# Performance work log

Hardware: AMD Instinct MI355X
Metric: run time of the kernel (lower is better)

The kernel has to match this reference:

```python
import jax, jax.numpy as jnp
import numpy as np

D_MODEL = 2048
NUM_HEADS = 16
HEAD_DIM = D_MODEL // NUM_HEADS  # 128
B, L = 2, 2048


def setup_inputs() -> dict:
    key = jax.random.key(0)
    ks = jax.random.split(key, 7)
    s = 0.02
    return {
        "x": jax.random.normal(ks[0], (B, L, D_MODEL), dtype=jnp.float32),
        "Wq_w": jax.random.normal(ks[1], (D_MODEL, D_MODEL), dtype=jnp.float32) * s,
        "Wq_b": jnp.zeros((D_MODEL,), dtype=jnp.float32),
        "Wk_w": jax.random.normal(ks[2], (HEAD_DIM, D_MODEL), dtype=jnp.float32) * s,
        "Wk_b": jnp.zeros((HEAD_DIM,), dtype=jnp.float32),
        "Wv_w": jax.random.normal(ks[3], (HEAD_DIM, D_MODEL), dtype=jnp.float32) * s,
        "Wv_b": jnp.zeros((HEAD_DIM,), dtype=jnp.float32),
    }


def reference(x, Wq_w, Wq_b, Wk_w, Wk_b, Wv_w, Wv_b):
    b, l, _ = x.shape
    # torch Linear: y = x @ W.T + b
    Q = (x @ Wq_w.T + Wq_b).reshape(b, l, NUM_HEADS, HEAD_DIM)  # [B,L,H,D]
    K = x @ Wk_w.T + Wk_b  # [B,L,D] single shared KV head (MQA)
    V = x @ Wv_w.T + Wv_b  # [B,L,D]
    scale = 1.0 / jnp.sqrt(jnp.float32(HEAD_DIM))
    # scores: [B,H,Lq,Lk]; K's head dim (size 1 in torch) broadcasts -> contract over d only
    scores = jnp.einsum("bqhd,bkd->bhqk", Q, K) * scale
    attn = jax.nn.softmax(scores, axis=-1)
    out = jnp.einsum("bhqk,bkd->bqhd", attn, V)  # [B,L,H,D]
    return out.reshape(b, l, D_MODEL)
```

## Files before the change

### kernel.cpp

```cpp
#include <hip/hip_runtime.h>
#include <hip/hip_bf16.h>


typedef unsigned short u16;
typedef unsigned int u32;
typedef __bf16 bf16x8 __attribute__((ext_vector_type(8)));
typedef float f32x16 __attribute__((ext_vector_type(16)));
typedef u16 u16x4 __attribute__((ext_vector_type(4)));
typedef u32 u32x4 __attribute__((ext_vector_type(4)));

#define MFMA32(a, b, c) __builtin_amdgcn_mfma_f32_32x32x16_bf16((a), (b), (c), 0, 0, 0)

__device__ __forceinline__ u16 f2bf(float f) {
  __hip_bfloat16 h = __float2bfloat16(f);
  return __builtin_bit_cast(u16, h);
}

__device__ __forceinline__ float fexp2(float x) {
#if __has_builtin(__builtin_amdgcn_exp2f)
  return __builtin_amdgcn_exp2f(x);
#else
  return exp2f(x);
#endif
}

__device__ __forceinline__ void cp16(const void* g, void* l) {
  __builtin_amdgcn_global_load_lds(
      (const __attribute__((address_space(1))) u32*)g,
      (__attribute__((address_space(3))) u32*)l, 16, 0, 0);
}

__device__ __forceinline__ f32x16 zero16() {
  f32x16 v;
#pragma unroll
  for (int i = 0; i < 16; ++i) v[i] = 0.f;
  return v;
}

__global__ __launch_bounds__(256) void k_convert(
    const float* __restrict__ x, const float* __restrict__ wq,
    const float* __restrict__ wk, const float* __restrict__ wv,
    u16* __restrict__ xb, u16* __restrict__ wqb,
    u16* __restrict__ wkb, u16* __restrict__ wvb) {
  int idx = blockIdx.x * 256 + threadIdx.x;
  for (int i = idx; i < 3276800; i += 524288) {
    float4 v; u16* dst;
    if (i < 2097152) {
      v = ((const float4*)x)[i]; dst = xb + (size_t)i * 4;
    } else if (i < 3145728) {
      int j = i - 2097152; v = ((const float4*)wq)[j]; dst = wqb + (size_t)j * 4;
    } else if (i < 3211264) {
      int j = i - 3145728; v = ((const float4*)wk)[j]; dst = wkb + (size_t)j * 4;
    } else {
      int j = i - 3211264; v = ((const float4*)wv)[j]; dst = wvb + (size_t)j * 4;
    }
    u16x4 o;
    o[0] = f2bf(v.x); o[1] = f2bf(v.y); o[2] = f2bf(v.z); o[3] = f2bf(v.w);
    *(u16x4*)dst = o;
  }
}

__global__ __launch_bounds__(256, 2) void k_gemm_qkv(
    const u16* __restrict__ xb, const u16* __restrict__ wqb,
    const u16* __restrict__ wkb, const u16* __restrict__ wvb,
    const float* __restrict__ bq, const float* __restrict__ bk, const float* __restrict__ bv,
    u16* __restrict__ qout, u16* __restrict__ kout, u16* __restrict__ vtout) {
  __shared__ __align__(16) u16 sh[36864];
  const int tid = threadIdx.x;
  const int w = tid >> 6, lane = tid & 63, ln = lane & 31, hi = lane >> 5;
  const int wr = w >> 1, wc = w & 1;
  const int m0 = blockIdx.x * 128;
  const int by = blockIdx.y;
  const int mode = (by < 16) ? 0 : (by - 15);
  const int n0loc = (mode == 0) ? by * 128 : 0;
  const u16* __restrict__ Bp = (mode == 0) ? wqb : (mode == 1 ? wkb : wvb);
  const u16* Arow = xb + (size_t)m0 * 2048;
  const u16* Brow = Bp + (size_t)n0loc * 2048;

  const u16* sb[9];
#pragma unroll
  for (int i = 0; i < 9; ++i) {
    int s = (w + i * 4) * 64 + lane;
    const u16* base; int r, c;
    if (s < 1152) { r = s / 9; c = s % 9; if (c > 7) c = 0; base = Arow; }
    else { int s2 = s - 1152; r = s2 / 9; c = s2 % 9; if (c > 7) c = 0; base = Brow; }
    sb[i] = base + (size_t)r * 2048 + c * 8;
  }

  f32x16 acc[2][2];
  acc[0][0] = zero16(); acc[0][1] = zero16(); acc[1][0] = zero16(); acc[1][1] = zero16();

  const int a0off = (wr * 64 + ln) * 72 + hi * 8;
  const int b0off = 9216 + (wc * 64 + ln) * 72 + hi * 8;

#pragma unroll
  for (int i = 0; i < 9; ++i)
    cp16(sb[i], (void*)(sh + (w + i * 4) * 512));
  __syncthreads();

  for (int it = 0; it < 32; ++it) {
    const int cur = (it & 1) * 18432;
    const int nxt = 18432 - cur;
    const int k0n = (it < 31) ? (it + 1) * 64 : 0;
#pragma unroll
    for (int i = 0; i < 9; ++i)
      cp16(sb[i] + k0n, (void*)(sh + nxt + (w + i * 4) * 512));

#pragma unroll
    for (int kc = 0; kc < 4; ++kc) {
      const int ko = kc * 16;
      bf16x8 a0 = *(const bf16x8*)&sh[cur + a0off + ko];
      bf16x8 a1 = *(const bf16x8*)&sh[cur + a0off + 2304 + ko];
      bf16x8 b0 = *(const bf16x8*)&sh[cur + b0off + ko];
      bf16x8 b1 = *(const bf16x8*)&sh[cur + b0off + 2304 + ko];
      acc[0][0] = MFMA32(a0, b0, acc[0][0]);
      acc[0][1] = MFMA32(a0, b1, acc[0][1]);
      acc[1][0] = MFMA32(a1, b0, acc[1][0]);
      acc[1][1] = MFMA32(a1, b1, acc[1][1]);
    }

    __syncthreads();
  }

  const float qscale = 0.12751744630098356f;
#pragma unroll
  for (int fm = 0; fm < 2; ++fm) {
#pragma unroll
    for (int fn = 0; fn < 2; ++fn) {
      f32x16 a = acc[fm][fn];
      const int mbase = m0 + wr * 64 + fm * 32;
      const int nloc = n0loc + wc * 64 + fn * 32 + ln;
      if (mode == 0) {
        const float bsc = bq[nloc] * qscale;
#pragma unroll
        for (int r = 0; r < 16; ++r) {
          int row = (r & 3) + 8 * (r >> 2) + 4 * hi;
          qout[(size_t)(mbase + row) * 2048 + nloc] = f2bf(a[r] * qscale + bsc);
        }
      } else if (mode == 1) {
        const float bb = bk[nloc];
#pragma unroll
        for (int r = 0; r < 16; ++r) {
          int row = (r & 3) + 8 * (r >> 2) + 4 * hi;
          kout[(size_t)(mbase + row) * 128 + nloc] = f2bf(a[r] + bb);
        }
      } else {
        const float bb = bv[nloc];
#pragma unroll
        for (int r = 0; r < 16; ++r) {
          int row = (r & 3) + 8 * (r >> 2) + 4 * hi;
          int m = mbase + row;
          vtout[(size_t)((m >> 11) * 128 + nloc) * 2048 + (m & 2047)] = f2bf(a[r] + bb);
        }
      }
    }
  }
}

__global__ __launch_bounds__(512, 2) void k_attn(
    const u16* __restrict__ qb, const u16* __restrict__ kb, const u16* __restrict__ vtb,
    float* __restrict__ out) {
  __shared__ __align__(16) u16 sh[35840];
  const int tid = threadIdx.x;
  const int w = tid >> 6, lane = tid & 63, ln = lane & 31, hi = lane >> 5;
  const int q0 = blockIdx.x * 256, h = blockIdx.y, b = blockIdx.z;
  const size_t bL = (size_t)b * 2048;
  const u16* kbase = kb + bL * 128;
  const u16* vbase = vtb + (size_t)b * 128 * 2048;

  bf16x8 qf[8];
  {
    const u16* qrow = qb + (bL + q0 + w * 32 + ln) * 2048 + h * 128 + hi * 8;
#pragma unroll
    for (int kc = 0; kc < 8; ++kc) qf[kc] = *(const bf16x8*)(qrow + kc * 16);
  }

  const u16* sb[5]; int smul[5];
  const int nsl = (w < 3) ? 5 : 4;
#pragma unroll
  for (int i = 0; i < 5; ++i) {
    int sl = w + i * 8;
    if (sl < 35) {
      int s = sl * 64 + lane;
      if (s < 1088) {
        int r = s / 17, c = s % 17; if (c > 15) c = 0;
        sb[i] = kbase + r * 128 + c * 8; smul[i] = 128;
      } else {
        int s2 = s - 1088; int r = s2 / 9, c = s2 % 9; if (c > 7) c = 0;
        sb[i] = vbase + (size_t)r * 2048 + c * 8; smul[i] = 1;
      }
    } else { sb[i] = kbase; smul[i] = 0; }
  }

#pragma unroll
  for (int i = 0; i < 5; ++i)
    if (i < nsl) cp16(sb[i], (void*)(sh + (w + i * 8) * 512));
  __syncthreads();

  f32x16 o[4];
#pragma unroll
  for (int dg = 0; dg < 4; ++dg) o[dg] = zero16();
  float l = 0.f;

  const int kro = ln * 136 + hi * 8;
  const int vro = 8704 + ln * 72 + hi * 8;

  for (int it = 0; it < 32; ++it) {
    const int cur = (it & 1) * 17920;
    const int nxt = 17920 - cur;
    const size_t k0n = (it < 31) ? (size_t)(it + 1) * 64 : 0;
#pragma unroll
    for (int i = 0; i < 5; ++i)
      if (i < nsl) cp16(sb[i] + k0n * smul[i], (void*)(sh + nxt + (w + i * 8) * 512));

    f32x16 s0 = zero16(), s1 = zero16();
#pragma unroll
    for (int kc = 0; kc < 8; ++kc) {
      bf16x8 a0 = *(const bf16x8*)&sh[cur + kro + kc * 16];
      bf16x8 a1 = *(const bf16x8*)&sh[cur + kro + 32 * 136 + kc * 16];
      s0 = MFMA32(a0, qf[kc], s0);
      s1 = MFMA32(a1, qf[kc], s1);
    }

    u32 pk[16];
#pragma unroll
    for (int i = 0; i < 8; ++i) {
      float a = fexp2(s0[2 * i]), c = fexp2(s0[2 * i + 1]);
      pk[i] = __builtin_amdgcn_perm(__builtin_bit_cast(u32, c),
                                    __builtin_bit_cast(u32, a), 0x07060302u);
      float d = fexp2(s1[2 * i]), e = fexp2(s1[2 * i + 1]);
      pk[8 + i] = __builtin_amdgcn_perm(__builtin_bit_cast(u32, e),
                                        __builtin_bit_cast(u32, d), 0x07060302u);
    }
#pragma unroll
    for (int i = 0; i < 16; ++i) {
      l += __builtin_bit_cast(float, pk[i] << 16);
      l += __builtin_bit_cast(float, pk[i] & 0xffff0000u);
    }

    bf16x8 pf[4];
#pragma unroll
    for (int c = 0; c < 4; ++c) {
      const int wb = 4 * c;
      u32 send0 = hi ? pk[wb] : pk[wb + 2];
      u32 send1 = hi ? pk[wb + 1] : pk[wb + 3];
      u32 r0 = (u32)__shfl_xor((int)send0, 32, 64);
      u32 r1 = (u32)__shfl_xor((int)send1, 32, 64);
      u32x4 v;
      v[0] = hi ? r0 : pk[wb];
      v[1] = hi ? r1 : pk[wb + 1];
      v[2] = hi ? pk[wb + 2] : r0;
      v[3] = hi ? pk[wb + 3] : r1;
      pf[c] = __builtin_bit_cast(bf16x8, v);
    }

#pragma unroll
    for (int c = 0; c < 4; ++c)
#pragma unroll
      for (int dg = 0; dg < 4; ++dg) {
        bf16x8 va = *(const bf16x8*)&sh[cur + vro + dg * 2304 + c * 16];
        o[dg] = MFMA32(va, pf[c], o[dg]);
      }

    __syncthreads();
  }

  l += __shfl_xor(l, 32, 64);
  const float inv = 1.0f / l;

  float* orow = out + (bL + q0 + w * 32 + ln) * 2048 + h * 128 + hi * 4;
#pragma unroll
  for (int dg = 0; dg < 4; ++dg)
#pragma unroll
    for (int rq = 0; rq < 4; ++rq) {
      float4 v4;
      v4.x = o[dg][rq * 4 + 0] * inv; v4.y = o[dg][rq * 4 + 1] * inv;
      v4.z = o[dg][rq * 4 + 2] * inv; v4.w = o[dg][rq * 4 + 3] * inv;
      *(float4*)&orow[dg * 32 + rq * 8] = v4;
    }
}

extern "C" void kernel_launch(void* const* d_in, const int* in_sizes, int n_in,
                              void* d_out, int out_size, void* d_ws, size_t ws_size,
                              hipStream_t stream) {
  const float* x  = (const float*)d_in[0];
  const float* wq = (const float*)d_in[1];
  const float* bq = (const float*)d_in[2];
  const float* wk = (const float*)d_in[3];
  const float* bk = (const float*)d_in[4];
  const float* wv = (const float*)d_in[5];
  const float* bv = (const float*)d_in[6];
  float* out = (float*)d_out;
  char* ws = (char*)d_ws;

  u16* xb   = (u16*)(ws);
  u16* wqb  = (u16*)(ws + 16777216);
  u16* wkb  = (u16*)(ws + 25165824);
  u16* wvb  = (u16*)(ws + 25690112);
  u16* qb   = (u16*)(ws + 26214400);
  u16* kbuf = (u16*)(ws + 42991616);
  u16* vtb  = (u16*)(ws + 44040192);

  k_convert<<<2048, 256, 0, stream>>>(x, wq, wk, wv, xb, wqb, wkb, wvb);
  k_gemm_qkv<<<dim3(32, 18), 256, 0, stream>>>(xb, wqb, wkb, wvb, bq, bk, bv, qb, kbuf, vtb);
  k_attn<<<dim3(8, 16, 2), 512, 0, stream>>>(qb, kbuf, vtb, out);
}
```

Baseline: 229.5 us.

## Halve attention block size, add MFMA priority hints, use permlane32 swap and packed bf16 convert

The attention kernel now launches 256-thread blocks covering 128 query rows each, with twice as many blocks, and each wave issues more cp16 loads to fill the shared K/V tile. s_setprio raises wave priority around the MFMA loops in both the QKV GEMM and attention kernels so matrix issue is favoured over other waves. Softmax packing switches to v_cvt_pk_bf16_f32, which rounds instead of truncating, and the row sum now accumulates the fp32 exponentials rather than the truncated bf16 values. The cross-half shuffle becomes v_permlane32_swap. Smaller blocks mean each K/V tile load to LDS serves fewer queries, trading that extra load traffic for better scheduling flexibility.

```diff
diff --git a/kernel.cpp b/kernel.cpp
--- a/kernel.cpp
+++ b/kernel.cpp
@@ -106,6 +106,7 @@
     for (int i = 0; i < 9; ++i)
       cp16(sb[i] + k0n, (void*)(sh + nxt + (w + i * 4) * 512));
 
+    __builtin_amdgcn_s_setprio(1);
 #pragma unroll
     for (int kc = 0; kc < 4; ++kc) {
       const int ko = kc * 16;
@@ -118,6 +119,7 @@
       acc[1][0] = MFMA32(a1, b0, acc[1][0]);
       acc[1][1] = MFMA32(a1, b1, acc[1][1]);
     }
+    __builtin_amdgcn_s_setprio(0);
 
     __syncthreads();
   }
@@ -157,13 +159,13 @@
   }
 }
 
-__global__ __launch_bounds__(512, 2) void k_attn(
+__global__ __launch_bounds__(256, 2) void k_attn(
     const u16* __restrict__ qb, const u16* __restrict__ kb, const u16* __restrict__ vtb,
     float* __restrict__ out) {
   __shared__ __align__(16) u16 sh[35840];
   const int tid = threadIdx.x;
   const int w = tid >> 6, lane = tid & 63, ln = lane & 31, hi = lane >> 5;
-  const int q0 = blockIdx.x * 256, h = blockIdx.y, b = blockIdx.z;
+  const int q0 = blockIdx.x * 128, h = blockIdx.y, b = blockIdx.z;
   const size_t bL = (size_t)b * 2048;
   const u16* kbase = kb + bL * 128;
   const u16* vbase = vtb + (size_t)b * 128 * 2048;
@@ -175,11 +177,11 @@
     for (int kc = 0; kc < 8; ++kc) qf[kc] = *(const bf16x8*)(qrow + kc * 16);
   }
 
-  const u16* sb[5]; int smul[5];
-  const int nsl = (w < 3) ? 5 : 4;
-#pragma unroll
-  for (int i = 0; i < 5; ++i) {
-    int sl = w + i * 8;
+  const u16* sb[9]; int smul[9];
+  const int nsl = (38 - w) >> 2;
+#pragma unroll
+  for (int i = 0; i < 9; ++i) {
+    int sl = w + i * 4;
     if (sl < 35) {
       int s = sl * 64 + lane;
       if (s < 1088) {
@@ -193,8 +195,8 @@
   }
 
 #pragma unroll
-  for (int i = 0; i < 5; ++i)
-    if (i < nsl) cp16(sb[i], (void*)(sh + (w + i * 8) * 512));
+  for (int i = 0; i < 9; ++i)
+    if (i < nsl) cp16(sb[i], (void*)(sh + (w + i * 4) * 512));
   __syncthreads();
 
   f32x16 o[4];
@@ -210,10 +212,11 @@
     const int nxt = 17920 - cur;
     const size_t k0n = (it < 31) ? (size_t)(it + 1) * 64 : 0;
 #pragma unroll
-    for (int i = 0; i < 5; ++i)
-      if (i < nsl) cp16(sb[i] + k0n * smul[i], (void*)(sh + nxt + (w + i * 8) * 512));
+    for (int i = 0; i < 9; ++i)
+      if (i < nsl) cp16(sb[i] + k0n * smul[i], (void*)(sh + nxt + (w + i * 4) * 512));
 
     f32x16 s0 = zero16(), s1 = zero16();
+    __builtin_amdgcn_s_setprio(1);
 #pragma unroll
     for (int kc = 0; kc < 8; ++kc) {
       bf16x8 a0 = *(const bf16x8*)&sh[cur + kro + kc * 16];
@@ -221,39 +224,33 @@
       s0 = MFMA32(a0, qf[kc], s0);
       s1 = MFMA32(a1, qf[kc], s1);
     }
+    __builtin_amdgcn_s_setprio(0);
 
     u32 pk[16];
 #pragma unroll
     for (int i = 0; i < 8; ++i) {
-      float a = fexp2(s0[2 * i]), c = fexp2(s0[2 * i + 1]);
-      pk[i] = __builtin_amdgcn_perm(__builtin_bit_cast(u32, c),
-                                    __builtin_bit_cast(u32, a), 0x07060302u);
-      float d = fexp2(s1[2 * i]), e = fexp2(s1[2 * i + 1]);
-      pk[8 + i] = __builtin_amdgcn_perm(__builtin_bit_cast(u32, e),
-                                        __builtin_bit_cast(u32, d), 0x07060302u);
-    }
-#pragma unroll
-    for (int i = 0; i < 16; ++i) {
-      l += __builtin_bit_cast(float, pk[i] << 16);
-      l += __builtin_bit_cast(float, pk[i] & 0xffff0000u);
+      float ea = fexp2(s0[2 * i]), eb = fexp2(s0[2 * i + 1]);
+      float ec = fexp2(s1[2 * i]), ed = fexp2(s1[2 * i + 1]);
+      u32 p0, p1;
+      asm("v_cvt_pk_bf16_f32 %0, %1, %2" : "=v"(p0) : "v"(ea), "v"(eb));
+      asm("v_cvt_pk_bf16_f32 %0, %1, %2" : "=v"(p1) : "v"(ec), "v"(ed));
+      pk[i] = p0; pk[8 + i] = p1;
+      l += (ea + eb) + (ec + ed);
     }
 
     bf16x8 pf[4];
 #pragma unroll
     for (int c = 0; c < 4; ++c) {
       const int wb = 4 * c;
-      u32 send0 = hi ? pk[wb] : pk[wb + 2];
-      u32 send1 = hi ? pk[wb + 1] : pk[wb + 3];
-      u32 r0 = (u32)__shfl_xor((int)send0, 32, 64);
-      u32 r1 = (u32)__shfl_xor((int)send1, 32, 64);
-      u32x4 v;
-      v[0] = hi ? r0 : pk[wb];
-      v[1] = hi ? r1 : pk[wb + 1];
-      v[2] = hi ? pk[wb + 2] : r0;
-      v[3] = hi ? pk[wb + 3] : r1;
-      pf[c] = __builtin_bit_cast(bf16x8, v);
-    }
-
+      u32 x0 = pk[wb], y0 = pk[wb + 2];
+      u32 x1 = pk[wb + 1], y1 = pk[wb + 3];
+      asm("v_permlane32_swap_b32 %0, %1" : "+v"(x0), "+v"(y0));
+      asm("v_permlane32_swap_b32 %0, %1" : "+v"(x1), "+v"(y1));
+      u32x4 vv; vv[0] = x0; vv[1] = x1; vv[2] = y0; vv[3] = y1;
+      pf[c] = __builtin_bit_cast(bf16x8, vv);
+    }
+
+    __builtin_amdgcn_s_setprio(1);
 #pragma unroll
     for (int c = 0; c < 4; ++c)
 #pragma unroll
@@ -261,6 +258,7 @@
         bf16x8 va = *(const bf16x8*)&sh[cur + vro + dg * 2304 + c * 16];
         o[dg] = MFMA32(va, pf[c], o[dg]);
       }
+    __builtin_amdgcn_s_setprio(0);
 
     __syncthreads();
   }
@@ -303,5 +301,5 @@
 
   k_convert<<<2048, 256, 0, stream>>>(x, wq, wk, wv, xb, wqb, wkb, wvb);
   k_gemm_qkv<<<dim3(32, 18), 256, 0, stream>>>(xb, wqb, wkb, wvb, bq, bk, bv, qb, kbuf, vtb);
-  k_attn<<<dim3(8, 16, 2), 512, 0, stream>>>(qb, kbuf, vtb, out);
-}
+  k_attn<<<dim3(16, 16, 2), 256, 0, stream>>>(qb, kbuf, vtb, out);
+}
```

Result: slower. 234.2 us (+2.0%).
